# Kernel tuning notes

Measured on AMD Instinct MI355X. Metric: run time of the kernel, lower is better.

The kernel has to match this reference:

```python
import jax, jax.numpy as jnp
import numpy as np

N_WG = 512      # waveguides n
N_COL = 512     # mesh columns
M = N_WG // 2   # node slots per column (odd columns have one masked dummy)
N_NODE = N_COL * M
B = 8192        # batch of input fields
PI4 = np.pi / 4


def build_mesh_indices():
    """Rectangular (Clements-style) mesh: per-column (top, bottom, mask) arrays."""
    top = np.zeros((N_COL, M), np.int32)
    bottom = np.zeros((N_COL, M), np.int32)
    mask = np.zeros((N_COL, M), np.int32)
    for c in range(N_COL):
        if c % 2 == 0:
            t = np.arange(0, N_WG, 2, dtype=np.int32)
            top[c], bottom[c], mask[c] = t, t + 1, 1
        else:
            t = np.arange(1, N_WG - 1, 2, dtype=np.int32)
            k = len(t)
            top[c, :k], bottom[c, :k], mask[c, :k] = t, t + 1, 1
            # masked dummy slot uses otherwise-unused rows 0 and N_WG-1
            top[c, k:], bottom[c, k:] = 0, N_WG - 1
    return jnp.asarray(top), jnp.asarray(bottom), jnp.asarray(mask)


def setup_inputs() -> dict:
    key = jax.random.key(0)
    ks = jax.random.split(key, 6)
    top, bottom, mask = build_mesh_indices()
    return {
        "x": jax.random.normal(ks[0], (N_WG, B), dtype=jnp.float32),
        "thetas": 2 * np.pi * jax.random.uniform(ks[1], (N_NODE,), dtype=jnp.float32),
        "phis": 2 * np.pi * jax.random.uniform(ks[2], (N_NODE,), dtype=jnp.float32),
        "gammas": 2 * np.pi * jax.random.uniform(ks[3], (N_WG,), dtype=jnp.float32),
        "bs_errors": 0.01 * jax.random.normal(ks[4], (N_NODE, 2), dtype=jnp.float32),
        "loss_errors": -0.1 * jax.random.uniform(ks[5], (N_NODE, 2), dtype=jnp.float32),
        "top": top, "bottom": bottom, "mask": mask,
    }


def _dc_terms(bs_errors, loss_errors, side):
    """_parallel_dc: per-node directional-coupler 2x2 elements [N,4] complex."""
    ins = jnp.exp(jnp.log(10.0) * loss_errors[:, side] / 20.0)
    e = bs_errors[:, side]
    s, c = jnp.sin(PI4 + e), jnp.cos(PI4 + e)
    t11 = (ins * s).astype(jnp.complex64)
    t12 = ins * (1j * c)
    t21 = (1j * c).astype(jnp.complex64)
    t22 = s.astype(jnp.complex64)
    return jnp.stack([t11, t12, t21, t22], axis=-1)


def _transform(v, T, t, b, m):
    """_parallel_transform: masked 2x2 gather-multiply-scatter. T: [M,4] complex."""
    vt, vb = v[t], v[b]
    one_m = 1.0 - m
    s11 = (T[:, 0] * m + one_m)[:, None]
    s12 = (T[:, 1] * m)[:, None]
    s21 = (T[:, 2] * m)[:, None]
    s22 = (T[:, 3] * m + one_m)[:, None]
    return v.at[t].set(s11 * vt + s21 * vb).at[b].set(s12 * vt + s22 * vb)


def reference(x, thetas, phis, gammas, bs_errors, loss_errors, top, bottom, mask):
    # input gamma phase screen, then propagate through all mesh columns
    v = x.astype(jnp.complex64) * jnp.exp(1j * gammas)[:, None]          # [n, B]
    left = _dc_terms(bs_errors, loss_errors, 0).reshape(N_COL, M, 4)
    right = _dc_terms(bs_errors, loss_errors, 1).reshape(N_COL, M, 4)
    th = thetas.reshape(N_COL, M)
    ph = phis.reshape(N_COL, M)
    mf = mask.astype(jnp.float32)

    def column(v, xs):
        t, b, m, thc, phc, L, R = xs
        # PhaseStyle.TOP, forward: phi -> left DC -> theta -> right DC
        v = v.at[t].multiply(jnp.exp(1j * phc * m)[:, None])
        v = _transform(v, L, t, b, m)
        v = v.at[t].multiply(jnp.exp(1j * thc * m)[:, None])
        v = _transform(v, R, t, b, m)
        return v, None

    v, _ = jax.lax.scan(column, v, (top, bottom, mf, th, ph, left, right))
    return jnp.stack([v.real, v.imag])  # [2, n, B]
```

## Files before the change

### kernel.cpp

```cpp
#include <hip/hip_runtime.h>
#include <math.h>

#define BATCH 8192
#define NROW 512
#define NCOL 512
#define MNODE 256

typedef __attribute__((ext_vector_type(8))) short bf16x8;
typedef __attribute__((ext_vector_type(4))) float f32x4;

__device__ __forceinline__ short2 split1(float x) {
  unsigned u = __float_as_uint(x);
  short h = (short)(u >> 16);
  float r = x - __uint_as_float(u & 0xffff0000u);
  short l = (short)(__float_as_uint(r) >> 16);
  return make_short2(h, l);
}

__global__ __launch_bounds__(256) void precomp_kernel(
    const float* __restrict__ thetas, const float* __restrict__ phis,
    const float* __restrict__ bse, const float* __restrict__ lse,
    float4* __restrict__ pp) {
  int n = blockIdx.x * 256 + threadIdx.x;
  float th = thetas[n], ph = phis[n];
  float e0 = bse[2 * n + 0], e1 = bse[2 * n + 1];
  float l0 = lse[2 * n + 0], l1 = lse[2 * n + 1];
  const float K = 0.16609640474436813f;
  float ins0 = exp2f(l0 * K), ins1 = exp2f(l1 * K);
  const float PI4 = 0.7853981633974483f;
  float s0, c0, s1, c1, sp, cp, st, ct;
  sincosf(PI4 + e0, &s0, &c0);
  sincosf(PI4 + e1, &s1, &c1);
  sincosf(ph, &sp, &cp);
  sincosf(th, &st, &ct);
  float AL = ins0 * s0, C1L = c0, C2L = ins0 * c0, SL = s0;
  float AR = ins1 * s1, C1R = c1, C2R = ins1 * c1, SR = s1;
  float a11r = AL * cp,   a11i = AL * sp;
  float a12r = 0.f,       a12i = C1L;
  float a21r = -C2L * sp, a21i = C2L * cp;
  float a22r = SL,        a22i = 0.f;
  float b11r = a11r * ct - a11i * st, b11i = a11r * st + a11i * ct;
  float b12r = a12r * ct - a12i * st, b12i = a12r * st + a12i * ct;
  float n11r = AR * b11r - C1R * a21i;
  float n11i = AR * b11i + C1R * a21r;
  float n12r = AR * b12r - C1R * a22i;
  float n12i = AR * b12i + C1R * a22r;
  float n21r = -C2R * b11i + SR * a21r;
  float n21i =  C2R * b11r + SR * a21i;
  float n22r = -C2R * b12i + SR * a22r;
  float n22i =  C2R * b12r + SR * a22i;
  pp[2 * n + 0] = make_float4(n11r, n11i, n12r, n12i);
  pp[2 * n + 1] = make_float4(n21r, n21i, n22r, n22i);
}

__device__ __forceinline__ void proc_pair(float& vtr, float& vti, float& vbr, float& vbi,
                                          const float4 q0, const float4 q1) {
  float tr = q0.x * vtr - q0.y * vti + q0.z * vbr - q0.w * vbi;
  float ti = q0.x * vti + q0.y * vtr + q0.z * vbi + q0.w * vbr;
  float br = q1.x * vtr - q1.y * vti + q1.z * vbr - q1.w * vbi;
  float bi = q1.x * vti + q1.y * vtr + q1.z * vbi + q1.w * vbr;
  vtr = tr; vti = ti; vbr = br; vbi = bi;
}

__device__ __forceinline__ int swz(int b) { return b ^ ((b >> 3) & 7); }

__global__ __launch_bounds__(256) void compose_kernel(
    const float* __restrict__ gammas, const float4* __restrict__ pp,
    float* __restrict__ Tsegs, int pairs_per_seg) {
  __shared__ float4 buf[2][1024];
  __shared__ float ep[1024][5];

  const int tid  = threadIdx.x;
  const int lane = tid & 63;
  const int w    = tid >> 6;
  const int seg  = blockIdx.x >> 7;
  const int g    = blockIdx.x & 127;
  const int col  = g * 4 + w;
  const int colmin = g * 4;

  const float4* ps = pp + (size_t)seg * pairs_per_seg * 1024;
  float* T = Tsegs + (size_t)seg * (1024 * NROW);

  float vr[8], vi[8];
#pragma unroll
  for (int r = 0; r < 8; ++r) {
    const int row = lane * 8 + r;
    vr[r] = 0.f; vi[r] = 0.f;
    if (row == col) {
      if (seg == 0) {
        float sg, cg;
        sincosf(gammas[row], &sg, &cg);
        vr[r] = cg; vi[r] = sg;
      } else {
        vr[r] = 1.f;
      }
    }
  }

  {
    const int sw = swz(tid);
#pragma unroll
    for (int k = 0; k < 4; ++k)
      buf[0][256 * k + sw] = ps[256 * k + tid];
  }
  __syncthreads();

  const int Lc = col >> 3;

#pragma unroll 1
  for (int p = 0; p < pairs_per_seg; ++p) {
    const int b = p & 1;

    const int HA = (p >> 2) + 3;
    const bool act  = (lane >= Lc - HA)     && (lane <= Lc + HA);
    const bool wide = (lane >= Lc - HA - 1) && (lane <= Lc + HA + 1);

    float4 f0, f1, f2, f3;
    bool st0 = false, st1 = false;
    if (p < pairs_per_seg - 1) {
      const int slo = colmin - 2 * p - 50;
      const int shi = colmin + 2 * p + 53;
      st0 = (tid + 1 >= slo) && (tid <= shi);
      st1 = (tid + 257 >= slo) && (tid + 256 <= shi);
      const float4* src = ps + (size_t)(p + 1) * 1024;
      if (st0) { f0 = src[tid];       f2 = src[512 + tid]; }
      if (st1) { f1 = src[256 + tid]; f3 = src[768 + tid]; }
    }

    float4 pe[8], po[7], pu1;
    if (act) {
      const int base = 8 * lane;
      const int l7 = lane & 7;
#pragma unroll
      for (int j = 0; j < 8; ++j) pe[j] = buf[b][base + (j ^ l7)];
#pragma unroll
      for (int j = 0; j < 7; ++j) po[j] = buf[b][512 + base + (j ^ l7)];
      const int lm = (lane == 0) ? 0 : lane - 1;
      pu1 = buf[b][512 + 8 * lm + (7 ^ (lm & 7))];

#pragma unroll
      for (int k = 0; k < 4; ++k)
        proc_pair(vr[2 * k], vi[2 * k], vr[2 * k + 1], vi[2 * k + 1],
                  pe[2 * k], pe[2 * k + 1]);

#pragma unroll
      for (int k = 0; k < 3; ++k)
        proc_pair(vr[2 * k + 1], vi[2 * k + 1], vr[2 * k + 2], vi[2 * k + 2],
                  po[2 * k], po[2 * k + 1]);
    }

    float br = 0.f, bi = 0.f, tu = 0.f, tv = 0.f;
    if (wide) {
      br = __shfl_down(vr[0], 1, 64);
      bi = __shfl_down(vi[0], 1, 64);
      tu = __shfl_up(vr[7], 1, 64);
      tv = __shfl_up(vi[7], 1, 64);
    }
    if (act) {
      float nAr = po[6].x * vr[7] - po[6].y * vi[7] + po[6].z * br - po[6].w * bi;
      float nAi = po[6].x * vi[7] + po[6].y * vr[7] + po[6].z * bi + po[6].w * br;
      float nBr = pu1.x * tu - pu1.y * tv + pu1.z * vr[0] - pu1.w * vi[0];
      float nBi = pu1.x * tv + pu1.y * tu + pu1.z * vi[0] + pu1.w * vr[0];
      if (lane < 63) { vr[7] = nAr; vi[7] = nAi; }
      if (lane > 0)  { vr[0] = nBr; vi[0] = nBi; }
    }

    if (p < pairs_per_seg - 1) {
      const int sw = swz(tid);
      if (st0) { buf[1 - b][sw] = f0;       buf[1 - b][512 + sw] = f2; }
      if (st1) { buf[1 - b][256 + sw] = f1; buf[1 - b][768 + sw] = f3; }
    }
    __syncthreads();
  }

#pragma unroll
  for (int r = 0; r < 8; ++r) {
    ep[lane * 8 + r][w] = vr[r];
    ep[512 + lane * 8 + r][w] = vi[r];
  }
  __syncthreads();
#pragma unroll
  for (int k = 0; k < 4; ++k) {
    const int i = k * 256 + tid;
    *(float4*)(T + (size_t)i * NROW + g * 4) =
        make_float4(ep[i][0], ep[i][1], ep[i][2], ep[i][3]);
  }
}

__global__ __launch_bounds__(256) void merge_mfma(
    const float* __restrict__ A0, const float* __restrict__ B0, float* __restrict__ C0,
    const float* __restrict__ A1, const float* __restrict__ B1, float* __restrict__ C1) {
  const float* A = blockIdx.z ? A1 : A0;
  const float* B = blockIdx.z ? B1 : B0;
  float*       C = blockIdx.z ? C1 : C0;

  __shared__ short sAh[64 * 40], sAl[64 * 40];

  const int tid = threadIdx.x;
  const int lane = tid & 63;
  const int w = tid >> 6;
  const int bm = blockIdx.y * 64;
  const int bn = blockIdx.x * 64;
  const int wm = (w & 1) * 32;
  const int wn = (w >> 1) * 32;
  const int q = lane >> 4;
  const int l15 = lane & 15;

  const int sm = tid >> 2;
  const int sk = (tid & 3) * 8;

  f32x4 acc[2][2];
#pragma unroll
  for (int i = 0; i < 2; ++i)
#pragma unroll
    for (int j = 0; j < 2; ++j) acc[i][j] = (f32x4){0.f, 0.f, 0.f, 0.f};

#pragma unroll 1
  for (int k0 = 0; k0 < 1024; k0 += 32) {
    {
      const int gm = bm + sm;
      const int gk = k0 + sk;
      const int r = gm & 511;
      const bool top = gm < 512;
      const bool left = gk < 512;
      const int col = gk & 511;
      const float* src = (top == left) ? (A + (size_t)r * 512)
                                       : (A + (size_t)(512 + r) * 512);
      const float sgn = (top && !left) ? -1.f : 1.f;
      float4 v0 = *(const float4*)(src + col);
      float4 v1 = *(const float4*)(src + col + 4);
      float vv[8] = {v0.x, v0.y, v0.z, v0.w, v1.x, v1.y, v1.z, v1.w};
      short h[8], l[8];
#pragma unroll
      for (int i = 0; i < 8; ++i) {
        short2 s = split1(sgn * vv[i]);
        h[i] = s.x; l[i] = s.y;
      }
      __syncthreads();
      *(bf16x8*)&sAh[sm * 40 + sk] = *(bf16x8*)h;
      *(bf16x8*)&sAl[sm * 40 + sk] = *(bf16x8*)l;
      __syncthreads();
    }

    bf16x8 bh[2], bl[2];
#pragma unroll
    for (int nt = 0; nt < 2; ++nt) {
      const float* bp = B + (size_t)(k0 + q * 8) * 512 + bn + wn + nt * 16 + l15;
      short hh[8], ll[8];
#pragma unroll
      for (int j = 0; j < 8; ++j) {
        short2 s = split1(bp[(size_t)j * 512]);
        hh[j] = s.x; ll[j] = s.y;
      }
      bh[nt] = *(bf16x8*)hh;
      bl[nt] = *(bf16x8*)ll;
    }

    bf16x8 ah[2], al[2];
#pragma unroll
    for (int mt = 0; mt < 2; ++mt) {
      const int m = wm + mt * 16 + l15;
      ah[mt] = *(const bf16x8*)&sAh[m * 40 + q * 8];
      al[mt] = *(const bf16x8*)&sAl[m * 40 + q * 8];
    }

#pragma unroll
    for (int mt = 0; mt < 2; ++mt)
#pragma unroll
      for (int nt = 0; nt < 2; ++nt) {
        acc[mt][nt] = __builtin_amdgcn_mfma_f32_16x16x32_bf16(ah[mt], bh[nt], acc[mt][nt], 0, 0, 0);
        acc[mt][nt] = __builtin_amdgcn_mfma_f32_16x16x32_bf16(ah[mt], bl[nt], acc[mt][nt], 0, 0, 0);
        acc[mt][nt] = __builtin_amdgcn_mfma_f32_16x16x32_bf16(al[mt], bh[nt], acc[mt][nt], 0, 0, 0);
      }
  }

#pragma unroll
  for (int mt = 0; mt < 2; ++mt)
#pragma unroll
    for (int nt = 0; nt < 2; ++nt)
#pragma unroll
      for (int r = 0; r < 4; ++r) {
        const int gm = bm + wm + mt * 16 + q * 4 + r;
        const int gn = bn + wn + nt * 16 + l15;
        C[(size_t)gm * 512 + gn] = acc[mt][nt][r];
      }
}

__global__ __launch_bounds__(256) void xprep_kernel(
    const float* __restrict__ x, short* __restrict__ xp) {
  const int t = blockIdx.x * 256 + threadIdx.x;
  const int n = t & 8191;
  const int g = t >> 13;
  const float* src = x + (size_t)g * 8 * BATCH + n;
  short h[8], l[8];
#pragma unroll
  for (int j = 0; j < 8; ++j) {
    short2 s = split1(src[(size_t)j * BATCH]);
    h[j] = s.x; l[j] = s.y;
  }
  short* dst = xp + (size_t)t * 16;
  *(bf16x8*)dst = *(bf16x8*)h;
  *(bf16x8*)(dst + 8) = *(bf16x8*)l;
}

__global__ __launch_bounds__(256) void gemm_mfma_packed(
    const float* __restrict__ A, const short* __restrict__ xp,
    float* __restrict__ C) {
  __shared__ short sAh[64 * 40], sAl[64 * 40];

  const int tid = threadIdx.x;
  const int lane = tid & 63;
  const int w = tid >> 6;
  const int bm = blockIdx.y * 64;
  const int bn = blockIdx.x * 128;
  const int wm = (w & 1) * 32;
  const int wn = (w >> 1) * 64;
  const int q = lane >> 4;
  const int l15 = lane & 15;

  const int sm = tid >> 2;
  const int sk = (tid & 3) * 8;
  const float* Ap = A + (size_t)(bm + sm) * 512 + sk;

  f32x4 acc[2][4];
#pragma unroll
  for (int i = 0; i < 2; ++i)
#pragma unroll
    for (int j = 0; j < 4; ++j) acc[i][j] = (f32x4){0.f, 0.f, 0.f, 0.f};

  float4 pa[2];
  pa[0] = *(const float4*)(Ap);
  pa[1] = *(const float4*)(Ap + 4);

#pragma unroll 1
  for (int k0 = 0; k0 < 512; k0 += 32) {
    {
      short h[8], l[8];
#pragma unroll
      for (int i = 0; i < 8; ++i) {
        short2 s = split1(((const float*)pa)[i]);
        h[i] = s.x; l[i] = s.y;
      }
      __syncthreads();
      *(bf16x8*)&sAh[sm * 40 + sk] = *(bf16x8*)h;
      *(bf16x8*)&sAl[sm * 40 + sk] = *(bf16x8*)l;
      __syncthreads();
    }

    if (k0 + 32 < 512) {
      pa[0] = *(const float4*)(Ap + k0 + 32);
      pa[1] = *(const float4*)(Ap + k0 + 36);
    }

    const int kt = k0 >> 5;
    bf16x8 bh[4], bl[4];
#pragma unroll
    for (int nt = 0; nt < 4; ++nt) {
      const short* bp = xp + (((size_t)(kt * 4 + q)) * BATCH +
                              (bn + wn + nt * 16 + l15)) * 16;
      bh[nt] = *(const bf16x8*)bp;
      bl[nt] = *(const bf16x8*)(bp + 8);
    }

    bf16x8 ah[2], al[2];
#pragma unroll
    for (int mt = 0; mt < 2; ++mt) {
      const int m = wm + mt * 16 + l15;
      ah[mt] = *(const bf16x8*)&sAh[m * 40 + q * 8];
      al[mt] = *(const bf16x8*)&sAl[m * 40 + q * 8];
    }

#pragma unroll
    for (int mt = 0; mt < 2; ++mt)
#pragma unroll
      for (int nt = 0; nt < 4; ++nt) {
        acc[mt][nt] = __builtin_amdgcn_mfma_f32_16x16x32_bf16(ah[mt], bh[nt], acc[mt][nt], 0, 0, 0);
        acc[mt][nt] = __builtin_amdgcn_mfma_f32_16x16x32_bf16(ah[mt], bl[nt], acc[mt][nt], 0, 0, 0);
        acc[mt][nt] = __builtin_amdgcn_mfma_f32_16x16x32_bf16(al[mt], bh[nt], acc[mt][nt], 0, 0, 0);
      }
  }

#pragma unroll
  for (int mt = 0; mt < 2; ++mt)
#pragma unroll
    for (int nt = 0; nt < 4; ++nt)
#pragma unroll
      for (int r = 0; r < 4; ++r) {
        const int gm = bm + wm + mt * 16 + q * 4 + r;
        const int gn = bn + wn + nt * 16 + l15;
        C[(size_t)gm * BATCH + gn] = acc[mt][nt][r];
      }
}

__global__ __launch_bounds__(256) void gemm_mfma(
    const float* __restrict__ A, const float* __restrict__ B,
    float* __restrict__ C) {
  __shared__ short sAh[128 * 40], sAl[128 * 40];

  const int tid = threadIdx.x;
  const int lane = tid & 63;
  const int w = tid >> 6;
  const int bm = blockIdx.y * 128;
  const int bn = blockIdx.x * 128;
  const int wm = (w & 1) * 64;
  const int wn = (w >> 1) * 64;
  const int q = lane >> 4;
  const int l15 = lane & 15;

  const int sm = tid >> 1;
  const int sk = (tid & 1) * 16;
  const float* Ap = A + (size_t)(bm + sm) * 512 + sk;

  f32x4 acc[4][4];
#pragma unroll
  for (int i = 0; i < 4; ++i)
#pragma unroll
    for (int j = 0; j < 4; ++j) acc[i][j] = (f32x4){0.f, 0.f, 0.f, 0.f};

  float4 pa[4];
#pragma unroll
  for (int i = 0; i < 4; ++i) pa[i] = *(const float4*)(Ap + i * 4);

#pragma unroll 1
  for (int k0 = 0; k0 < 512; k0 += 32) {
    {
      short h[16], l[16];
#pragma unroll
      for (int i = 0; i < 16; ++i) {
        short2 s = split1(((const float*)pa)[i]);
        h[i] = s.x; l[i] = s.y;
      }
      __syncthreads();
      *(bf16x8*)&sAh[sm * 40 + sk]     = *(bf16x8*)&h[0];
      *(bf16x8*)&sAh[sm * 40 + sk + 8] = *(bf16x8*)&h[8];
      *(bf16x8*)&sAl[sm * 40 + sk]     = *(bf16x8*)&l[0];
      *(bf16x8*)&sAl[sm * 40 + sk + 8] = *(bf16x8*)&l[8];
      __syncthreads();
    }

    if (k0 + 32 < 512) {
#pragma unroll
      for (int i = 0; i < 4; ++i) pa[i] = *(const float4*)(Ap + k0 + 32 + i * 4);
    }

    bf16x8 bh[4], bl[4];
#pragma unroll
    for (int nt = 0; nt < 4; ++nt) {
      const float* bp = B + (size_t)(k0 + q * 8) * BATCH + bn + wn + nt * 16 + l15;
      short hh[8], ll[8];
#pragma unroll
      for (int j = 0; j < 8; ++j) {
        short2 s = split1(bp[(size_t)j * BATCH]);
        hh[j] = s.x; ll[j] = s.y;
      }
      bh[nt] = *(bf16x8*)hh;
      bl[nt] = *(bf16x8*)ll;
    }

    bf16x8 ah[4], al[4];
#pragma unroll
    for (int mt = 0; mt < 4; ++mt) {
      const int m = wm + mt * 16 + l15;
      ah[mt] = *(const bf16x8*)&sAh[m * 40 + q * 8];
      al[mt] = *(const bf16x8*)&sAl[m * 40 + q * 8];
    }

#pragma unroll
    for (int mt = 0; mt < 4; ++mt)
#pragma unroll
      for (int nt = 0; nt < 4; ++nt) {
        acc[mt][nt] = __builtin_amdgcn_mfma_f32_16x16x32_bf16(ah[mt], bh[nt], acc[mt][nt], 0, 0, 0);
        acc[mt][nt] = __builtin_amdgcn_mfma_f32_16x16x32_bf16(ah[mt], bl[nt], acc[mt][nt], 0, 0, 0);
        acc[mt][nt] = __builtin_amdgcn_mfma_f32_16x16x32_bf16(al[mt], bh[nt], acc[mt][nt], 0, 0, 0);
      }
  }

#pragma unroll
  for (int mt = 0; mt < 4; ++mt)
#pragma unroll
    for (int nt = 0; nt < 4; ++nt)
#pragma unroll
      for (int r = 0; r < 4; ++r) {
        const int gm = bm + wm + mt * 16 + q * 4 + r;
        const int gn = bn + wn + nt * 16 + l15;
        C[(size_t)gm * BATCH + gn] = acc[mt][nt][r];
      }
}

extern "C" void kernel_launch(void* const* d_in, const int* in_sizes, int n_in,
                              void* d_out, int out_size, void* d_ws, size_t ws_size,
                              hipStream_t stream) {
  const float* x      = (const float*)d_in[0];
  const float* thetas = (const float*)d_in[1];
  const float* phis   = (const float*)d_in[2];
  const float* gammas = (const float*)d_in[3];
  const float* bse    = (const float*)d_in[4];
  const float* lse    = (const float*)d_in[5];

  float* base = (float*)d_ws;
  float4* pp  = (float4*)d_ws;
  const size_t PPF   = 1048576;
  const size_t SEGSZ = 524288;

  precomp_kernel<<<512, 256, 0, stream>>>(thetas, phis, bse, lse, pp);

  if (ws_size >= (size_t)24 * 1024 * 1024) {
    float* segs = base + PPF;
    compose_kernel<<<512, 256, 0, stream>>>(gammas, pp, segs, 64);

    float* T0  = segs + 0 * SEGSZ;
    float* T1  = segs + 1 * SEGSZ;
    float* T2  = segs + 2 * SEGSZ;
    float* T3  = segs + 3 * SEGSZ;
    float* T10 = segs + 4 * SEGSZ;
    float* T32 = segs + 5 * SEGSZ;
    float* Tf  = base;
    merge_mfma<<<dim3(8, 16, 2), 256, 0, stream>>>(T1, T0, T10, T3, T2, T32);
    merge_mfma<<<dim3(8, 16, 1), 256, 0, stream>>>(T32, T10, Tf, T32, T10, Tf);

    short* xp = (short*)(base + SEGSZ);
    xprep_kernel<<<2048, 256, 0, stream>>>(x, xp);

    gemm_mfma_packed<<<dim3(64, 16), 256, 0, stream>>>(Tf, xp, (float*)d_out);
  } else {
    int nseg;
    if (ws_size >= (size_t)14 * 1024 * 1024)      nseg = 4;
    else if (ws_size >= (size_t)8 * 1024 * 1024)  nseg = 2;
    else                                          nseg = 1;

    float* segs = base + PPF;
    float* Tf;
    compose_kernel<<<nseg * 128, 256, 0, stream>>>(gammas, pp, segs, 256 / nseg);

    if (nseg == 4) {
      float* T0  = segs + 0 * SEGSZ;
      float* T1  = segs + 1 * SEGSZ;
      float* T2  = segs + 2 * SEGSZ;
      float* T3  = segs + 3 * SEGSZ;
      float* T10 = base;
      float* T32 = base + SEGSZ;
      Tf = segs + 4 * SEGSZ;
      merge_mfma<<<dim3(8, 16, 2), 256, 0, stream>>>(T1, T0, T10, T3, T2, T32);
      merge_mfma<<<dim3(8, 16, 1), 256, 0, stream>>>(T32, T10, Tf, T32, T10, Tf);
    } else if (nseg == 2) {
      float* T0 = segs + 0 * SEGSZ;
      float* T1 = segs + 1 * SEGSZ;
      Tf = base;
      merge_mfma<<<dim3(8, 16, 1), 256, 0, stream>>>(T1, T0, Tf, T1, T0, Tf);
    } else {
      Tf = segs;
    }

    gemm_mfma<<<dim3(BATCH / 128, 8), 256, 0, stream>>>(Tf, x, (float*)d_out);
  }
}
```

Baseline: 266.8 us.

## Split mesh into eight segments and skip zero bands in merge GEMMs

Compose now builds eight 32-pair segment transfer matrices instead of four, and a three-level tree of merge GEMMs combines them. The new merge kernel uses the banded structure of each segment matrix (half-bandwidth HA/HB) to limit the K loop to the nonzero range for each output tile, skipping zero blocks. The compose epilogue reuses the double-buffer shared memory instead of a separate array, which lowers LDS use and may raise occupancy. The risks are extra launches, and wrong results if the stated bandwidths underestimate the true nonzero band.

```diff
diff --git a/kernel.cpp b/kernel.cpp
--- a/kernel.cpp
+++ b/kernel.cpp
@@ -68,7 +68,7 @@
     const float* __restrict__ gammas, const float4* __restrict__ pp,
     float* __restrict__ Tsegs, int pairs_per_seg) {
   __shared__ float4 buf[2][1024];
-  __shared__ float ep[1024][5];
+  float* epf = (float*)buf;
 
   const int tid  = threadIdx.x;
   const int lane = tid & 63;
@@ -175,24 +175,24 @@
 
 #pragma unroll
   for (int r = 0; r < 8; ++r) {
-    ep[lane * 8 + r][w] = vr[r];
-    ep[512 + lane * 8 + r][w] = vi[r];
+    epf[(lane * 8 + r) * 5 + w] = vr[r];
+    epf[(512 + lane * 8 + r) * 5 + w] = vi[r];
   }
   __syncthreads();
 #pragma unroll
   for (int k = 0; k < 4; ++k) {
     const int i = k * 256 + tid;
     *(float4*)(T + (size_t)i * NROW + g * 4) =
-        make_float4(ep[i][0], ep[i][1], ep[i][2], ep[i][3]);
-  }
-}
-
-__global__ __launch_bounds__(256) void merge_mfma(
-    const float* __restrict__ A0, const float* __restrict__ B0, float* __restrict__ C0,
-    const float* __restrict__ A1, const float* __restrict__ B1, float* __restrict__ C1) {
-  const float* A = blockIdx.z ? A1 : A0;
-  const float* B = blockIdx.z ? B1 : B0;
-  float*       C = blockIdx.z ? C1 : C0;
+        make_float4(epf[i * 5 + 0], epf[i * 5 + 1], epf[i * 5 + 2], epf[i * 5 + 3]);
+  }
+}
+
+__global__ __launch_bounds__(256) void merge_g(
+    const float* __restrict__ Ab, const float* __restrict__ Bb,
+    float* __restrict__ Cb, long sA, long sB, long sC, int HA, int HB) {
+  const float* A = Ab + (long)blockIdx.z * sA;
+  const float* B = Bb + (long)blockIdx.z * sB;
+  float*       C = Cb + (long)blockIdx.z * sC;
 
   __shared__ short sAh[64 * 40], sAl[64 * 40];
 
@@ -209,69 +209,90 @@
   const int sm = tid >> 2;
   const int sk = (tid & 3) * 8;
 
+  const int rmin = (blockIdx.y & 7) * 64;
+  int klo = rmin - HA;
+  {
+    int t = bn - HB;
+    if (t > klo) klo = t;
+    if (klo < 0) klo = 0;
+  }
+  int khi = rmin + 63 + HA;
+  {
+    int t = bn + 63 + HB;
+    if (t < khi) khi = t;
+    if (khi > 511) khi = 511;
+  }
+  klo &= ~31;
+
   f32x4 acc[2][2];
 #pragma unroll
   for (int i = 0; i < 2; ++i)
 #pragma unroll
     for (int j = 0; j < 2; ++j) acc[i][j] = (f32x4){0.f, 0.f, 0.f, 0.f};
 
+  if (klo <= khi) {
 #pragma unroll 1
-  for (int k0 = 0; k0 < 1024; k0 += 32) {
-    {
-      const int gm = bm + sm;
-      const int gk = k0 + sk;
-      const int r = gm & 511;
-      const bool top = gm < 512;
-      const bool left = gk < 512;
-      const int col = gk & 511;
-      const float* src = (top == left) ? (A + (size_t)r * 512)
-                                       : (A + (size_t)(512 + r) * 512);
-      const float sgn = (top && !left) ? -1.f : 1.f;
-      float4 v0 = *(const float4*)(src + col);
-      float4 v1 = *(const float4*)(src + col + 4);
-      float vv[8] = {v0.x, v0.y, v0.z, v0.w, v1.x, v1.y, v1.z, v1.w};
-      short h[8], l[8];
-#pragma unroll
-      for (int i = 0; i < 8; ++i) {
-        short2 s = split1(sgn * vv[i]);
-        h[i] = s.x; l[i] = s.y;
-      }
-      __syncthreads();
-      *(bf16x8*)&sAh[sm * 40 + sk] = *(bf16x8*)h;
-      *(bf16x8*)&sAl[sm * 40 + sk] = *(bf16x8*)l;
-      __syncthreads();
-    }
-
-    bf16x8 bh[2], bl[2];
-#pragma unroll
-    for (int nt = 0; nt < 2; ++nt) {
-      const float* bp = B + (size_t)(k0 + q * 8) * 512 + bn + wn + nt * 16 + l15;
-      short hh[8], ll[8];
-#pragma unroll
-      for (int j = 0; j < 8; ++j) {
-        short2 s = split1(bp[(size_t)j * 512]);
-        hh[j] = s.x; ll[j] = s.y;
-      }
-      bh[nt] = *(bf16x8*)hh;
-      bl[nt] = *(bf16x8*)ll;
-    }
-
-    bf16x8 ah[2], al[2];
-#pragma unroll
-    for (int mt = 0; mt < 2; ++mt) {
-      const int m = wm + mt * 16 + l15;
-      ah[mt] = *(const bf16x8*)&sAh[m * 40 + q * 8];
-      al[mt] = *(const bf16x8*)&sAl[m * 40 + q * 8];
-    }
-
-#pragma unroll
-    for (int mt = 0; mt < 2; ++mt)
-#pragma unroll
-      for (int nt = 0; nt < 2; ++nt) {
-        acc[mt][nt] = __builtin_amdgcn_mfma_f32_16x16x32_bf16(ah[mt], bh[nt], acc[mt][nt], 0, 0, 0);
-        acc[mt][nt] = __builtin_amdgcn_mfma_f32_16x16x32_bf16(ah[mt], bl[nt], acc[mt][nt], 0, 0, 0);
-        acc[mt][nt] = __builtin_amdgcn_mfma_f32_16x16x32_bf16(al[mt], bh[nt], acc[mt][nt], 0, 0, 0);
-      }
+    for (int h = 0; h < 2; ++h) {
+#pragma unroll 1
+      for (int k0 = klo; k0 <= khi; k0 += 32) {
+        const int gkb = h * 512 + k0;
+        {
+          const int gm = bm + sm;
+          const int gk = gkb + sk;
+          const int r = gm & 511;
+          const bool top = gm < 512;
+          const bool left = gk < 512;
+          const int col = gk & 511;
+          const float* src = (top == left) ? (A + (size_t)r * 512)
+                                           : (A + (size_t)(512 + r) * 512);
+          const float sgn = (top && !left) ? -1.f : 1.f;
+          float4 v0 = *(const float4*)(src + col);
+          float4 v1 = *(const float4*)(src + col + 4);
+          float vv[8] = {v0.x, v0.y, v0.z, v0.w, v1.x, v1.y, v1.z, v1.w};
+          short hh[8], ll[8];
+#pragma unroll
+          for (int i = 0; i < 8; ++i) {
+            short2 s = split1(sgn * vv[i]);
+            hh[i] = s.x; ll[i] = s.y;
+          }
+          __syncthreads();
+          *(bf16x8*)&sAh[sm * 40 + sk] = *(bf16x8*)hh;
+          *(bf16x8*)&sAl[sm * 40 + sk] = *(bf16x8*)ll;
+          __syncthreads();
+        }
+
+        bf16x8 bh[2], bl[2];
+#pragma unroll
+        for (int nt = 0; nt < 2; ++nt) {
+          const float* bp = B + (size_t)(gkb + q * 8) * 512 + bn + wn + nt * 16 + l15;
+          short hh[8], ll[8];
+#pragma unroll
+          for (int j = 0; j < 8; ++j) {
+            short2 s = split1(bp[(size_t)j * 512]);
+            hh[j] = s.x; ll[j] = s.y;
+          }
+          bh[nt] = *(bf16x8*)hh;
+          bl[nt] = *(bf16x8*)ll;
+        }
+
+        bf16x8 ah[2], al[2];
+#pragma unroll
+        for (int mt = 0; mt < 2; ++mt) {
+          const int m = wm + mt * 16 + l15;
+          ah[mt] = *(const bf16x8*)&sAh[m * 40 + q * 8];
+          al[mt] = *(const bf16x8*)&sAl[m * 40 + q * 8];
+        }
+
+#pragma unroll
+        for (int mt = 0; mt < 2; ++mt)
+#pragma unroll
+          for (int nt = 0; nt < 2; ++nt) {
+            acc[mt][nt] = __builtin_amdgcn_mfma_f32_16x16x32_bf16(ah[mt], bh[nt], acc[mt][nt], 0, 0, 0);
+            acc[mt][nt] = __builtin_amdgcn_mfma_f32_16x16x32_bf16(ah[mt], bl[nt], acc[mt][nt], 0, 0, 0);
+            acc[mt][nt] = __builtin_amdgcn_mfma_f32_16x16x32_bf16(al[mt], bh[nt], acc[mt][nt], 0, 0, 0);
+          }
+      }
+    }
   }
 
 #pragma unroll
@@ -499,26 +520,31 @@
 
   float* base = (float*)d_ws;
   float4* pp  = (float4*)d_ws;
-  const size_t PPF   = 1048576;
-  const size_t SEGSZ = 524288;
+  const long PPF   = 1048576;
+  const long S     = 524288;
 
   precomp_kernel<<<512, 256, 0, stream>>>(thetas, phis, bse, lse, pp);
 
   if (ws_size >= (size_t)24 * 1024 * 1024) {
     float* segs = base + PPF;
-    compose_kernel<<<512, 256, 0, stream>>>(gammas, pp, segs, 64);
-
-    float* T0  = segs + 0 * SEGSZ;
-    float* T1  = segs + 1 * SEGSZ;
-    float* T2  = segs + 2 * SEGSZ;
-    float* T3  = segs + 3 * SEGSZ;
-    float* T10 = segs + 4 * SEGSZ;
-    float* T32 = segs + 5 * SEGSZ;
-    float* Tf  = base;
-    merge_mfma<<<dim3(8, 16, 2), 256, 0, stream>>>(T1, T0, T10, T3, T2, T32);
-    merge_mfma<<<dim3(8, 16, 1), 256, 0, stream>>>(T32, T10, Tf, T32, T10, Tf);
-
-    short* xp = (short*)(base + SEGSZ);
+    compose_kernel<<<1024, 256, 0, stream>>>(gammas, pp, segs, 32);
+
+    float* U0 = base + 5 * PPF;
+    float* U1 = base + 5 * PPF + S;
+    float* U2 = base;
+    float* U3 = base + S;
+    merge_g<<<dim3(8, 16, 2), 256, 0, stream>>>(
+        segs + S, segs, U0, 2 * S, 2 * S, S, 68, 68);
+    merge_g<<<dim3(8, 16, 2), 256, 0, stream>>>(
+        segs + 5 * S, segs + 4 * S, U2, 2 * S, 2 * S, S, 68, 68);
+    float* V0 = base + PPF;
+    float* V1 = base + PPF + S;
+    merge_g<<<dim3(8, 16, 2), 256, 0, stream>>>(
+        U1, U0, V0, (long)(U3 - U1), (long)(U2 - U0), S, 136, 136);
+    float* Tf = base;
+    merge_g<<<dim3(8, 16, 1), 256, 0, stream>>>(V1, V0, Tf, 0, 0, 0, 272, 272);
+
+    short* xp = (short*)(base + S);
     xprep_kernel<<<2048, 256, 0, stream>>>(x, xp);
 
     gemm_mfma_packed<<<dim3(64, 16), 256, 0, stream>>>(Tf, xp, (float*)d_out);
@@ -533,20 +559,17 @@
     compose_kernel<<<nseg * 128, 256, 0, stream>>>(gammas, pp, segs, 256 / nseg);
 
     if (nseg == 4) {
-      float* T0  = segs + 0 * SEGSZ;
-      float* T1  = segs + 1 * SEGSZ;
-      float* T2  = segs + 2 * SEGSZ;
-      float* T3  = segs + 3 * SEGSZ;
       float* T10 = base;
-      float* T32 = base + SEGSZ;
-      Tf = segs + 4 * SEGSZ;
-      merge_mfma<<<dim3(8, 16, 2), 256, 0, stream>>>(T1, T0, T10, T3, T2, T32);
-      merge_mfma<<<dim3(8, 16, 1), 256, 0, stream>>>(T32, T10, Tf, T32, T10, Tf);
+      float* T32 = base + S;
+      Tf = segs + 4 * S;
+      merge_g<<<dim3(8, 16, 2), 256, 0, stream>>>(
+          segs + S, segs, T10, 2 * S, 2 * S, S, 132, 132);
+      merge_g<<<dim3(8, 16, 1), 256, 0, stream>>>(
+          T32, T10, Tf, 0, 0, 0, 264, 264);
     } else if (nseg == 2) {
-      float* T0 = segs + 0 * SEGSZ;
-      float* T1 = segs + 1 * SEGSZ;
       Tf = base;
-      merge_mfma<<<dim3(8, 16, 1), 256, 0, stream>>>(T1, T0, Tf, T1, T0, Tf);
+      merge_g<<<dim3(8, 16, 1), 256, 0, stream>>>(
+          segs + S, segs, Tf, 0, 0, 0, 260, 260);
     } else {
       Tf = segs;
     }
```

After: 262.8 us. About the same (-1.5%).
